# Performance work log

Measured on AMD Instinct MI355X. Metric: run time of the kernel, lower is better.

The kernel has to match this reference:

```python
import jax, jax.numpy as jnp
import numpy as np

# Module config: point_dim=2, channels_in=16, channels_out=16, mlp_channels=[8,8], use_bias=False
# set_quad(24) -> N=24 Gauss-Legendre points per axis, decay_param=(24/4)**4
# set_output_locs(12) -> 12x12=144 output locations
N_QUAD = 24
M_SIDE = 12
CI = 16
CO = 16
HID = 8
PDIM = 2
BATCH = 32
DECAY = (N_QUAD / 4.0) ** 4  # 1296.0


def setup_inputs() -> dict:
    key = jax.random.key(0)
    ks = jax.random.split(key, 4)
    # Gauss-Legendre quadrature (glpair equivalent)
    qn, qw = np.polynomial.legendre.leggauss(N_QUAD)
    quad_nodes = jnp.asarray(qn, jnp.float32)
    quad_weights = jnp.asarray(qw, jnp.float32)
    # set_output_locs(M_SIDE): meshgrid('xy') of M_SIDE Gauss nodes, row k=i*m+j -> (n_j, n_i)
    on, _ = np.polynomial.legendre.leggauss(M_SIDE)
    on = jnp.asarray(on, jnp.float32)
    output_locs = jnp.stack([jnp.tile(on, M_SIDE), jnp.repeat(on, M_SIDE)], axis=-1)  # (144, 2)
    features = jax.random.normal(ks[0], (BATCH, CI, N_QUAD * N_QUAD), jnp.float32)
    # One Sin-MLP (2->8->8->1, no bias) per (out,in) channel pair; torch Linear init U(-1/sqrt(fan_in), +)
    def lin(k, fi, fo):
        b = 1.0 / np.sqrt(fi)
        return jax.random.uniform(k, (CO, CI, fi, fo), jnp.float32, -b, b)
    W1 = lin(ks[1], PDIM, HID)
    W2 = lin(ks[2], HID, HID)
    W3 = lin(ks[3], HID, 1)
    return dict(features=features, output_locs=output_locs, quad_nodes=quad_nodes,
                quad_weights=quad_weights, W1=W1, W2=W2, W3=W3)


def _forward(features, output_locs, quad_nodes, quad_weights, W1, W2, W3):
    n = quad_nodes.shape[0]
    # rquad(level=2) flattened: feature index k = i*n + j maps to node (n_j, n_i), weight w_i*w_j
    nodes2d = jnp.stack([jnp.tile(quad_nodes, n), jnp.repeat(quad_nodes, n)], axis=-1)  # (K, 2)
    w2d = jnp.repeat(quad_weights, n) * jnp.tile(quad_weights, n)                      # (K,)
    x = output_locs[:, None, :] - nodes2d[None, :, :]   # (M, K, 2) kernel eval offsets
    M, K, _ = x.shape
    xf = x.reshape(M * K, PDIM)                          # (P, 2), P = M*K
    # eval_MLPs: grouped tiny MLPs over all (out,in) pairs, Sin activations
    h = jnp.sin(jnp.einsum('pd,ocdh->ocph', xf, W1))     # (CO, CI, P, HID)
    h = jnp.sin(jnp.einsum('ocph,ochg->ocpg', h, W2))    # (CO, CI, P, HID)
    w = jnp.einsum('ocpg,ocg->ocp', h, W3[..., 0])       # (CO, CI, P)
    # bump: e * exp(-1/(1 - decay*||x||^4)) inside compact support, 0 outside
    da = DECAY * jnp.sum(xf * xf, axis=-1) ** 2          # decay * ||x||^4, (P,)
    inside = da < 1.0
    den = jnp.where(inside, 1.0 - da, 1.0)
    bump = jnp.where(inside, jnp.float32(np.e) * jnp.exp(-1.0 / den), 0.0)
    mesh_w = jnp.tile(w2d, M)                            # per p = m*K + k -> w2d[k]
    kern = (w * bump * mesh_w).reshape(CO, CI, M, K)
    # quadrature contraction over input channels and quadrature points
    return jnp.einsum('ocmk,bck->bom', kern, features)   # (B, CO, M)


def reference(features, output_locs, quad_nodes, quad_weights, W1, W2, W3):
    return _forward(features, output_locs, quad_nodes, quad_weights, W1, W2, W3)
```

## Files before the change

### kernel.cpp

```cpp
#include <hip/hip_runtime.h>
#include <math.h>


#define NQ 24
#define M_TOT 144
#define NB 32

__device__ __forceinline__ float sin_poly(float x) {
    float z = x * x;
    float r = fmaf(z, 2.7557313707070068e-06f, -1.9841269659586510e-04f);
    r = fmaf(z, r, 8.3333333332248946e-03f);
    r = fmaf(z, r, -1.6666666666666632e-01f);
    return fmaf(x * z, r, x);
}

__global__ __launch_bounds__(256, 2)
void quadconv_kernel(const float* __restrict__ F,
                     const float* __restrict__ OL,
                     const float* __restrict__ QN,
                     const float* __restrict__ QW,
                     const float* __restrict__ W1,
                     const float* __restrict__ W2,
                     const float* __restrict__ W3,
                     float* __restrict__ OUT) {
    const int ik = blockIdx.x;
    const int m  = blockIdx.y;
    const int t  = threadIdx.x;
    const int o  = t >> 4;
    const int c  = t & 15;

    const float oy = OL[2 * m + 1];
    const float x1 = oy - QN[ik];
    const float x1sq = x1 * x1;
    if (x1sq >= 1.0f / 36.0f) return;

    const float ox   = OL[2 * m];
    const float qwik = QW[ik];

    __shared__ float f_s[NQ * 512];
    __shared__ float qn_s[NQ], qw_s[NQ];

    if (t < NQ) { qn_s[t] = QN[t]; qw_s[t] = QW[t]; }

    float w1r[16], w2r[64], w3r[8];
    {
        const float4* p1 = (const float4*)(W1 + t * 16);
        #pragma unroll
        for (int i = 0; i < 4; ++i) ((float4*)w1r)[i] = p1[i];
        const float4* p2 = (const float4*)(W2 + t * 64);
        #pragma unroll
        for (int i = 0; i < 16; ++i) ((float4*)w2r)[i] = p2[i];
        const float4* p3 = (const float4*)(W3 + t * 8);
        #pragma unroll
        for (int i = 0; i < 2; ++i) ((float4*)w3r)[i] = p3[i];
    }

    {
        const int kbase = ik * NQ;
        #pragma unroll
        for (int pp = 0; pp < 2; ++pp) {
            const int p  = t + pp * 256;
            const int b  = p >> 4;
            const int cc = p & 15;
            const float4* src = (const float4*)(F + b * 9216 + cc * 576 + kbase);
            float4 q[6];
            #pragma unroll
            for (int j = 0; j < 6; ++j) q[j] = src[j];
            const float* qs = (const float*)q;
            #pragma unroll
            for (int j = 0; j < NQ; ++j) f_s[j * 512 + p] = qs[j];
        }
    }
    __syncthreads();

    float acc[NB];
    #pragma unroll
    for (int b = 0; b < NB; ++b) acc[b] = 0.0f;
    bool any = false;

    for (int jk = 0; jk < NQ; ++jk) {
        float x0 = ox - qn_s[jk];
        float r2 = fmaf(x0, x0, x1sq);
        float da = 1296.0f * r2 * r2;
        if (da >= 1.0f) continue;
        any = true;

        float bump = 2.718281828459045f * expf(-1.0f / (1.0f - da));
        float kscale = bump * qwik * qw_s[jk];

        float h1[8];
        #pragma unroll
        for (int h = 0; h < 8; ++h)
            h1[h] = sin_poly(fmaf(x0, w1r[h], x1 * w1r[8 + h]));

        float wsum = 0.0f;
        #pragma unroll
        for (int g = 0; g < 8; ++g) {
            float z = h1[0] * w2r[g];
            #pragma unroll
            for (int h = 1; h < 8; ++h)
                z = fmaf(h1[h], w2r[h * 8 + g], z);
            wsum = fmaf(sin_poly(z), w3r[g], wsum);
        }

        float kv = wsum * kscale;
        const float* fp = &f_s[jk * 512 + c];
        #pragma unroll
        for (int b = 0; b < NB; ++b)
            acc[b] = fmaf(kv, fp[b * 16], acc[b]);
    }

    if (!any) return;

    #pragma unroll
    for (int b = 0; b < NB; ++b) {
        float v = acc[b];
        v += __shfl_xor(v, 1);
        v += __shfl_xor(v, 2);
        v += __shfl_xor(v, 4);
        v += __shfl_xor(v, 8);
        acc[b] = v;
    }
    if (c == 0) {
        #pragma unroll
        for (int b = 0; b < NB; ++b)
            atomicAdd(&OUT[b * (16 * M_TOT) + o * M_TOT + m], acc[b]);
    }
}

extern "C" void kernel_launch(void* const* d_in, const int* in_sizes, int n_in,
                              void* d_out, int out_size, void* d_ws, size_t ws_size,
                              hipStream_t stream) {
    const float* F  = (const float*)d_in[0];
    const float* OL = (const float*)d_in[1];
    const float* QN = (const float*)d_in[2];
    const float* QW = (const float*)d_in[3];
    const float* W1 = (const float*)d_in[4];
    const float* W2 = (const float*)d_in[5];
    const float* W3 = (const float*)d_in[6];
    float* OUT = (float*)d_out;
    hipMemsetAsync(d_out, 0, (size_t)out_size * sizeof(float), stream);
    quadconv_kernel<<<dim3(NQ, M_TOT), dim3(256), 0, stream>>>(F, OL, QN, QW, W1, W2, W3, OUT);
}
```

Baseline: 94.26 us.

## Collapse grid to one block per output location and drop atomics and memset

```diff
diff --git a/kernel.cpp b/kernel.cpp
--- a/kernel.cpp
+++ b/kernel.cpp
@@ -23,23 +23,12 @@
                      const float* __restrict__ W2,
                      const float* __restrict__ W3,
                      float* __restrict__ OUT) {
-    const int ik = blockIdx.x;
-    const int m  = blockIdx.y;
-    const int t  = threadIdx.x;
-    const int o  = t >> 4;
-    const int c  = t & 15;
+    const int m = blockIdx.x;
+    const int t = threadIdx.x;
+    const int o = t >> 4;
+    const int c = t & 15;
 
-    const float oy = OL[2 * m + 1];
-    const float x1 = oy - QN[ik];
-    const float x1sq = x1 * x1;
-    if (x1sq >= 1.0f / 36.0f) return;
-
-    const float ox   = OL[2 * m];
-    const float qwik = QW[ik];
-
-    __shared__ float f_s[NQ * 512];
     __shared__ float qn_s[NQ], qw_s[NQ];
-
     if (t < NQ) { qn_s[t] = QN[t]; qw_s[t] = QW[t]; }
 
     float w1r[16], w2r[64], w3r[8];
@@ -54,63 +43,54 @@
         #pragma unroll
         for (int i = 0; i < 2; ++i) ((float4*)w3r)[i] = p3[i];
     }
+    __syncthreads();
 
-    {
-        const int kbase = ik * NQ;
-        #pragma unroll
-        for (int pp = 0; pp < 2; ++pp) {
-            const int p  = t + pp * 256;
-            const int b  = p >> 4;
-            const int cc = p & 15;
-            const float4* src = (const float4*)(F + b * 9216 + cc * 576 + kbase);
-            float4 q[6];
-            #pragma unroll
-            for (int j = 0; j < 6; ++j) q[j] = src[j];
-            const float* qs = (const float*)q;
-            #pragma unroll
-            for (int j = 0; j < NQ; ++j) f_s[j * 512 + p] = qs[j];
-        }
-    }
-    __syncthreads();
+    const float ox = OL[2 * m];
+    const float oy = OL[2 * m + 1];
 
     float acc[NB];
     #pragma unroll
     for (int b = 0; b < NB; ++b) acc[b] = 0.0f;
-    bool any = false;
 
-    for (int jk = 0; jk < NQ; ++jk) {
-        float x0 = ox - qn_s[jk];
-        float r2 = fmaf(x0, x0, x1sq);
-        float da = 1296.0f * r2 * r2;
-        if (da >= 1.0f) continue;
-        any = true;
+    const float* __restrict__ Fc = F + c * 576;
 
-        float bump = 2.718281828459045f * expf(-1.0f / (1.0f - da));
-        float kscale = bump * qwik * qw_s[jk];
+    for (int ik = 0; ik < NQ; ++ik) {
+        const float x1 = oy - qn_s[ik];
+        const float x1sq = x1 * x1;
+        if (x1sq >= 1.0f / 36.0f) continue;
+        const float qwik = qw_s[ik];
 
-        float h1[8];
-        #pragma unroll
-        for (int h = 0; h < 8; ++h)
-            h1[h] = sin_poly(fmaf(x0, w1r[h], x1 * w1r[8 + h]));
+        for (int jk = 0; jk < NQ; ++jk) {
+            const float x0 = ox - qn_s[jk];
+            const float r2 = fmaf(x0, x0, x1sq);
+            const float da = 1296.0f * r2 * r2;
+            if (da >= 1.0f) continue;
 
-        float wsum = 0.0f;
-        #pragma unroll
-        for (int g = 0; g < 8; ++g) {
-            float z = h1[0] * w2r[g];
+            const float bump = 2.718281828459045f * expf(-1.0f / (1.0f - da));
+            const float kscale = bump * qwik * qw_s[jk];
+
+            float h1[8];
             #pragma unroll
-            for (int h = 1; h < 8; ++h)
-                z = fmaf(h1[h], w2r[h * 8 + g], z);
-            wsum = fmaf(sin_poly(z), w3r[g], wsum);
+            for (int h = 0; h < 8; ++h)
+                h1[h] = sin_poly(fmaf(x0, w1r[h], x1 * w1r[8 + h]));
+
+            float wsum = 0.0f;
+            #pragma unroll
+            for (int g = 0; g < 8; ++g) {
+                float z = h1[0] * w2r[g];
+                #pragma unroll
+                for (int h = 1; h < 8; ++h)
+                    z = fmaf(h1[h], w2r[h * 8 + g], z);
+                wsum = fmaf(sin_poly(z), w3r[g], wsum);
+            }
+
+            const float kv = wsum * kscale;
+            const float* __restrict__ fp = Fc + ik * NQ + jk;
+            #pragma unroll
+            for (int b = 0; b < NB; ++b)
+                acc[b] = fmaf(kv, fp[b * 9216], acc[b]);
         }
-
-        float kv = wsum * kscale;
-        const float* fp = &f_s[jk * 512 + c];
-        #pragma unroll
-        for (int b = 0; b < NB; ++b)
-            acc[b] = fmaf(kv, fp[b * 16], acc[b]);
     }
-
-    if (!any) return;
 
     #pragma unroll
     for (int b = 0; b < NB; ++b) {
@@ -124,7 +104,7 @@
     if (c == 0) {
         #pragma unroll
         for (int b = 0; b < NB; ++b)
-            atomicAdd(&OUT[b * (16 * M_TOT) + o * M_TOT + m], acc[b]);
+            OUT[b * (16 * M_TOT) + o * M_TOT + m] = acc[b];
     }
 }
 
@@ -139,6 +119,5 @@
     const float* W2 = (const float*)d_in[5];
     const float* W3 = (const float*)d_in[6];
     float* OUT = (float*)d_out;
-    hipMemsetAsync(d_out, 0, (size_t)out_size * sizeof(float), stream);
-    quadconv_kernel<<<dim3(NQ, M_TOT), dim3(256), 0, stream>>>(F, OL, QN, QW, W1, W2, W3, OUT);
+    quadconv_kernel<<<dim3(M_TOT), dim3(256), 0, stream>>>(F, OL, QN, QW, W1, W2, W3, OUT);
 }
```

New measurement: 165.4 us. 1.75x slower.
